# Kernel optimization log

Hardware: AMD Instinct MI355X
Metric: run time of the kernel (lower is better)

## Reference

```python
import jax, jax.numpy as jnp
import numpy as np

B, N, L, D = 128, 1024, 512, 64


def setup_inputs() -> dict:
    key = jax.random.key(0)
    k1, k2 = jax.random.split(key)
    text_outputs = jax.random.normal(k1, (B, N, D), dtype=jnp.float32)
    image_outputs = jax.random.normal(k2, (B, L, D), dtype=jnp.float32)
    rng = np.random.RandomState(0)
    ntok = rng.randint(N // 4, N + 1, size=B)
    nreg = rng.randint(L // 4, L + 1, size=B)
    text_mask = (np.arange(N)[None, :] < ntok[:, None]).astype(np.float32)
    image_mask = (np.arange(L)[None, :] < nreg[:, None]).astype(np.float32)
    # impostor indices (torch code samples these with np.random inside forward;
    # here they are fixed constants for determinism), guaranteed != own index
    I_imp = rng.randint(0, B, size=B)
    S_imp = rng.randint(0, B, size=B)
    ar = np.arange(B)
    I_imp = np.where(I_imp == ar, (I_imp + 1) % B, I_imp).astype(np.int32)
    S_imp = np.where(S_imp == ar, (S_imp + 1) % B, S_imp).astype(np.int32)
    return {
        "text_outputs": text_outputs,
        "image_outputs": image_outputs,
        "text_mask": jnp.asarray(text_mask),
        "image_mask": jnp.asarray(image_mask),
        "I_imp_idx": jnp.asarray(I_imp),
        "S_imp_idx": jnp.asarray(S_imp),
    }


def _mean_max_sim(T, I, tmask, imask):
    # T: (N, D) tokens, I: (L, D) regions; masks select the ragged valid prefix.
    M = jnp.einsum('nd,ld->nl', T, I)                       # matchmap (N, L)
    neg = jnp.finfo(M.dtype).min
    mx = jnp.max(jnp.where(imask[None, :] > 0, M, neg), axis=1)  # max over regions
    return jnp.sum(mx * tmask) / jnp.sum(tmask)             # mean over valid tokens


def reference(text_outputs, image_outputs, text_mask, image_mask, I_imp_idx, S_imp_idx, margin=1.0):
    sim = jax.vmap(_mean_max_sim)
    anchor = sim(text_outputs, image_outputs, text_mask, image_mask)            # (B,)
    Simpsim = sim(text_outputs[S_imp_idx], image_outputs, text_mask[S_imp_idx], image_mask)
    Iimpsim = sim(text_outputs, image_outputs[I_imp_idx], text_mask, image_mask[I_imp_idx])
    # scalar per-sample hinge: term added only when margin+imp-anchor > 0 == relu
    per_sample = jax.nn.relu(margin + Iimpsim - anchor) + jax.nn.relu(margin + Simpsim - anchor)
    loss = jnp.sum(per_sample) / text_outputs.shape[0]
    return loss[None]  # torch returns shape (1,)
```

## Files before the change

kernel.cpp:

```cpp
#include <hip/hip_runtime.h>
#include <hip/hip_bf16.h>

#define B 128
#define N 1024
#define L 512
#define D 64

typedef float f32x4 __attribute__((ext_vector_type(4)));
typedef short bf16x8 __attribute__((ext_vector_type(8)));

__device__ inline bf16x8 cvt8(float4 f0, float4 f1) {
    union { __hip_bfloat162 h2[4]; bf16x8 v; } u;
    u.h2[0] = __float22bfloat162_rn(make_float2(f0.x, f0.y));
    u.h2[1] = __float22bfloat162_rn(make_float2(f0.z, f0.w));
    u.h2[2] = __float22bfloat162_rn(make_float2(f1.x, f1.y));
    u.h2[3] = __float22bfloat162_rn(make_float2(f1.z, f1.w));
    return u.v;
}

__device__ __forceinline__ void gload16(const void* g, void* l) {
    __builtin_amdgcn_global_load_lds(
        (const __attribute__((address_space(1))) void*)g,
        (__attribute__((address_space(3))) void*)l, 16, 0, 0);
}

__global__ __launch_bounds__(256) void prep_kernel(
        const float* __restrict__ tmask, const float* __restrict__ imask,
        const float* __restrict__ I,
        int* __restrict__ counts, unsigned short* __restrict__ Ibf) {
    int blk = blockIdx.x, tid = threadIdx.x;
    if (blk < B) {
        int b = blk;
        int w = tid >> 6, lane = tid & 63;
        float ts = 0.f, is = 0.f;
        const float* tm = tmask + (size_t)b * N;
#pragma unroll
        for (int i = 0; i < N / 256; ++i) ts += tm[tid + i * 256];
        const float* im = imask + (size_t)b * L;
#pragma unroll
        for (int i = 0; i < L / 256; ++i) is += im[tid + i * 256];
        for (int off = 32; off; off >>= 1) {
            ts += __shfl_down(ts, off);
            is += __shfl_down(is, off);
        }
        __shared__ float red[8];
        if (lane == 0) { red[w] = ts; red[4 + w] = is; }
        __syncthreads();
        if (tid == 0) counts[b]     = (int)(red[0] + red[1] + red[2] + red[3] + 0.5f);
        if (tid == 1) counts[B + b] = (int)(red[4] + red[5] + red[6] + red[7] + 0.5f);
    } else {
        int t = (blk - B) * 256 + tid;
#pragma unroll
        for (int j = 0; j < 4; ++j) {
            size_t ci = (size_t)t + (size_t)j * 131072;
            const float4* p = (const float4*)(I + ci * 8);
            *(bf16x8*)(Ibf + ci * 8) = cvt8(p[0], p[1]);
        }
    }
}

__global__ __launch_bounds__(256, 4) void sim_kernel_bf16(
        const float* __restrict__ T, const unsigned short* __restrict__ Ibf,
        const int* __restrict__ counts,
        const int* __restrict__ Iimp, const int* __restrict__ Simp,
        float* __restrict__ partials) {
    int blk = blockIdx.x;
    int chunk = blk & 3;
    int bs = blk >> 2;
    int b = bs & (B - 1);
    int s = bs >> 7;
    int Tb = b, Ib = b;
    if (s == 1) Tb = Simp[b];
    else if (s == 2) Ib = Iimp[b];

    int tid = threadIdx.x;
    int w = tid >> 6;
    int lane = tid & 63;
    int q = lane >> 4;
    int c = lane & 15;

    int ntok = counts[Tb];
    int nreg = counts[B + Ib];

    int tok0 = chunk << 8;
    if (chunk != 0 && tok0 >= ntok) {
        if (tid == 0) partials[blk] = 0.f;
        return;
    }

    __shared__ unsigned short ldsI[3][4096];
    __shared__ float red[4];

    int wt0 = tok0 + w * 64;
    bf16x8 afrag[4][2];
#pragma unroll
    for (int tt = 0; tt < 4; ++tt) {
        const float* trow = T + ((size_t)Tb * N + wt0 + tt * 16 + c) * D;
#pragma unroll
        for (int h = 0; h < 2; ++h) {
            const float4* p = (const float4*)(trow + h * 32 + q * 8);
            afrag[tt][h] = cvt8(p[0], p[1]);
        }
    }

    float mx[4][4];
#pragma unroll
    for (int tt = 0; tt < 4; ++tt)
#pragma unroll
        for (int i = 0; i < 4; ++i) mx[tt][i] = -3.0e38f;

    int rloc[2], eoff[2];
#pragma unroll
    for (int j = 0; j < 2; ++j) {
        int ci = tid + j * 256;
        int g = ci >> 6, ln = ci & 63;
        rloc[j] = (g >> 1) * 16 + (ln & 15);
        eoff[j] = (g & 1) * 32 + (ln >> 4) * 8;
    }
    const unsigned short* Ibase = Ibf + (size_t)Ib * L * D;
    int nchunks = (nreg + 63) >> 6;
    int nregm1 = nreg - 1;

    auto stage = [&](int k) {
        unsigned short* buf = &ldsI[k % 3][0];
        int rbase = k << 6;
#pragma unroll
        for (int j = 0; j < 2; ++j) {
            int r = rbase + rloc[j];
            if (r > nregm1) r = nregm1;
            gload16(Ibase + (size_t)r * D + eoff[j], buf + (size_t)(tid + j * 256) * 8);
        }
    };

    asm volatile("s_waitcnt vmcnt(0)" ::: "memory");
    stage(0);
    stage(1);
    asm volatile("s_waitcnt vmcnt(2)" ::: "memory");
    __builtin_amdgcn_s_barrier();

    for (int k = 0; k < nchunks; ++k) {
        if (k + 2 < nchunks) stage(k + 2);

        const char* base = (const char*)&ldsI[k % 3][0] + (size_t)lane * 16;
#pragma unroll
        for (int rt = 0; rt < 4; ++rt) {
            bf16x8 b0 = *(const bf16x8*)(base + (rt * 2 + 0) * 1024);
            bf16x8 b1 = *(const bf16x8*)(base + (rt * 2 + 1) * 1024);
#pragma unroll
            for (int tt = 0; tt < 4; ++tt) {
                f32x4 acc = {0.f, 0.f, 0.f, 0.f};
                acc = __builtin_amdgcn_mfma_f32_16x16x32_bf16(afrag[tt][0], b0, acc, 0, 0, 0);
                acc = __builtin_amdgcn_mfma_f32_16x16x32_bf16(afrag[tt][1], b1, acc, 0, 0, 0);
#pragma unroll
                for (int i = 0; i < 4; ++i) mx[tt][i] = fmaxf(mx[tt][i], acc[i]);
            }
        }

        if (k + 1 < nchunks) {
            if (k + 2 < nchunks)
                asm volatile("s_waitcnt vmcnt(2) lgkmcnt(0)" ::: "memory");
            else
                asm volatile("s_waitcnt vmcnt(0) lgkmcnt(0)" ::: "memory");
            __builtin_amdgcn_s_barrier();
        }
    }

#pragma unroll
    for (int m = 1; m < 16; m <<= 1) {
#pragma unroll
        for (int tt = 0; tt < 4; ++tt)
#pragma unroll
            for (int i = 0; i < 4; ++i)
                mx[tt][i] = fmaxf(mx[tt][i], __shfl_xor(mx[tt][i], m));
    }

    float bsum = 0.f;
    if (c == 0) {
#pragma unroll
        for (int tt = 0; tt < 4; ++tt)
#pragma unroll
            for (int i = 0; i < 4; ++i) {
                int row = wt0 + tt * 16 + q * 4 + i;
                if (row < ntok) bsum += mx[tt][i];
            }
    }
    for (int off = 32; off; off >>= 1) bsum += __shfl_down(bsum, off);
    if (lane == 0) red[w] = bsum;
    __syncthreads();
    if (tid == 0)
        partials[blk] = (red[0] + red[1] + red[2] + red[3]) / (float)ntok;
}

__global__ __launch_bounds__(256) void count_kernel(
        const float* __restrict__ tmask, const float* __restrict__ imask,
        int* __restrict__ counts) {
    int b = blockIdx.x, tid = threadIdx.x;
    int w = tid >> 6, lane = tid & 63;
    float ts = 0.f, is = 0.f;
    const float* tm = tmask + (size_t)b * N;
#pragma unroll
    for (int i = 0; i < N / 256; ++i) ts += tm[tid + i * 256];
    const float* im = imask + (size_t)b * L;
#pragma unroll
    for (int i = 0; i < L / 256; ++i) is += im[tid + i * 256];
    for (int off = 32; off; off >>= 1) {
        ts += __shfl_down(ts, off);
        is += __shfl_down(is, off);
    }
    __shared__ float red[8];
    if (lane == 0) { red[w] = ts; red[4 + w] = is; }
    __syncthreads();
    if (tid == 0) counts[b]     = (int)(red[0] + red[1] + red[2] + red[3] + 0.5f);
    if (tid == 1) counts[B + b] = (int)(red[4] + red[5] + red[6] + red[7] + 0.5f);
}

__global__ __launch_bounds__(256, 3) void sim_kernel_f32(
        const float* __restrict__ T, const float* __restrict__ I,
        const int* __restrict__ counts,
        const int* __restrict__ Iimp, const int* __restrict__ Simp,
        float* __restrict__ partials) {
    int blk = blockIdx.x;
    int chunk = blk & 3;
    int bs = blk >> 2;
    int b = bs & (B - 1);
    int s = bs >> 7;
    int Tb = b, Ib = b;
    if (s == 1) Tb = Simp[b];
    else if (s == 2) Ib = Iimp[b];

    int tid = threadIdx.x;
    int w = tid >> 6;
    int lane = tid & 63;
    int q = lane >> 4;
    int c = lane & 15;

    int ntok = counts[Tb];
    int nreg = counts[B + Ib];

    int tok0 = chunk << 8;
    if (chunk != 0 && tok0 >= ntok) {
        if (tid == 0) partials[blk] = 0.f;
        return;
    }

    __shared__ float ldsI[3][4096];
    __shared__ float red[4];

    int wt0 = tok0 + w * 64;
    bf16x8 afrag[4][2];
#pragma unroll
    for (int tt = 0; tt < 4; ++tt) {
        const float* trow = T + ((size_t)Tb * N + wt0 + tt * 16 + c) * D;
#pragma unroll
        for (int h = 0; h < 2; ++h) {
            const float4* p = (const float4*)(trow + h * 32 + q * 8);
            afrag[tt][h] = cvt8(p[0], p[1]);
        }
    }

    float mx[4][4];
#pragma unroll
    for (int tt = 0; tt < 4; ++tt)
#pragma unroll
        for (int i = 0; i < 4; ++i) mx[tt][i] = -3.0e38f;

    int rloc[4], foff[4];
#pragma unroll
    for (int j = 0; j < 4; ++j) {
        int ci = tid + j * 256;
        int fh = ci >> 7, idx = ci & 127, half = idx >> 6, ln2 = idx & 63;
        rloc[j] = (fh >> 1) * 16 + (ln2 & 15);
        foff[j] = (fh & 1) * 32 + (ln2 >> 4) * 8 + half * 4;
    }
    const float* Ibase = I + (size_t)Ib * L * D;
    int nchunks = (nreg + 63) >> 6;
    int nregm1 = nreg - 1;

    auto stage = [&](int k) {
        float* buf = &ldsI[k % 3][0];
        int rbase = k << 6;
#pragma unroll
        for (int j = 0; j < 4; ++j) {
            int r = rbase + rloc[j];
            if (r > nregm1) r = nregm1;
            gload16(Ibase + (size_t)r * D + foff[j], buf + (tid + j * 256) * 4);
        }
    };

    asm volatile("s_waitcnt vmcnt(0)" ::: "memory");
    stage(0);
    stage(1);
    asm volatile("s_waitcnt vmcnt(4)" ::: "memory");
    __builtin_amdgcn_s_barrier();

    for (int k = 0; k < nchunks; ++k) {
        if (k + 2 < nchunks) stage(k + 2);

        const char* base = (const char*)&ldsI[k % 3][0] + (size_t)lane * 16;
#pragma unroll
        for (int rt = 0; rt < 4; ++rt) {
            float4 e0 = *(const float4*)(base + (rt * 2 + 0) * 2048);
            float4 e1 = *(const float4*)(base + (rt * 2 + 0) * 2048 + 1024);
            float4 e2 = *(const float4*)(base + (rt * 2 + 1) * 2048);
            float4 e3 = *(const float4*)(base + (rt * 2 + 1) * 2048 + 1024);
            bf16x8 b0 = cvt8(e0, e1);
            bf16x8 b1 = cvt8(e2, e3);
#pragma unroll
            for (int tt = 0; tt < 4; ++tt) {
                f32x4 acc = {0.f, 0.f, 0.f, 0.f};
                acc = __builtin_amdgcn_mfma_f32_16x16x32_bf16(afrag[tt][0], b0, acc, 0, 0, 0);
                acc = __builtin_amdgcn_mfma_f32_16x16x32_bf16(afrag[tt][1], b1, acc, 0, 0, 0);
#pragma unroll
                for (int i = 0; i < 4; ++i) mx[tt][i] = fmaxf(mx[tt][i], acc[i]);
            }
        }

        if (k + 1 < nchunks) {
            if (k + 2 < nchunks)
                asm volatile("s_waitcnt vmcnt(4) lgkmcnt(0)" ::: "memory");
            else
                asm volatile("s_waitcnt vmcnt(0) lgkmcnt(0)" ::: "memory");
            __builtin_amdgcn_s_barrier();
        }
    }

#pragma unroll
    for (int m = 1; m < 16; m <<= 1) {
#pragma unroll
        for (int tt = 0; tt < 4; ++tt)
#pragma unroll
            for (int i = 0; i < 4; ++i)
                mx[tt][i] = fmaxf(mx[tt][i], __shfl_xor(mx[tt][i], m));
    }

    float bsum = 0.f;
    if (c == 0) {
#pragma unroll
        for (int tt = 0; tt < 4; ++tt)
#pragma unroll
            for (int i = 0; i < 4; ++i) {
                int row = wt0 + tt * 16 + q * 4 + i;
                if (row < ntok) bsum += mx[tt][i];
            }
    }
    for (int off = 32; off; off >>= 1) bsum += __shfl_down(bsum, off);
    if (lane == 0) red[w] = bsum;
    __syncthreads();
    if (tid == 0)
        partials[blk] = (red[0] + red[1] + red[2] + red[3]) / (float)ntok;
}

__global__ void loss_kernel(const float* __restrict__ partials,
                            float* __restrict__ out) {
    int tid = threadIdx.x;
    __shared__ float simsL[384];
    __shared__ float w6[6];
    const float4* p4 = (const float4*)partials;
    float4 v = p4[tid];
    simsL[tid] = v.x + v.y + v.z + v.w;
    __syncthreads();
    float per = 0.f;
    if (tid < B) {
        float anc  = simsL[tid];
        float simp = simsL[B + tid];
        float iimp = simsL[2 * B + tid];
        per = fmaxf(1.f + iimp - anc, 0.f) + fmaxf(1.f + simp - anc, 0.f);
    }
    for (int off = 32; off; off >>= 1) per += __shfl_down(per, off);
    if ((tid & 63) == 0) w6[tid >> 6] = per;
    __syncthreads();
    if (tid == 0)
        out[0] = (w6[0] + w6[1] + w6[2] + w6[3] + w6[4] + w6[5]) / (float)B;
}

extern "C" void kernel_launch(void* const* d_in, const int* in_sizes, int n_in,
                              void* d_out, int out_size, void* d_ws, size_t ws_size,
                              hipStream_t stream) {
    const float* T     = (const float*)d_in[0];
    const float* I     = (const float*)d_in[1];
    const float* tmask = (const float*)d_in[2];
    const float* imask = (const float*)d_in[3];
    const int*   Iimp  = (const int*)d_in[4];
    const int*   Simp  = (const int*)d_in[5];
    int*   counts   = (int*)d_ws;
    float* partials = (float*)((char*)d_ws + 1024);
    size_t need_bf16 = 7168 + (size_t)B * L * D * sizeof(unsigned short);

    if (ws_size >= need_bf16) {
        unsigned short* Ibf = (unsigned short*)((char*)d_ws + 7168);
        prep_kernel<<<B + 512, 256, 0, stream>>>(tmask, imask, I, counts, Ibf);
        sim_kernel_bf16<<<3 * B * 4, 256, 0, stream>>>(T, Ibf, counts, Iimp, Simp, partials);
    } else {
        count_kernel<<<B, 256, 0, stream>>>(tmask, imask, counts);
        sim_kernel_f32<<<3 * B * 4, 256, 0, stream>>>(T, I, counts, Iimp, Simp, partials);
    }
    loss_kernel<<<1, 384, 0, stream>>>(partials, (float*)d_out);
}
```

Baseline: 122.1 us.

## Fuse loss reduction into sim kernel via last-block atomic and remap block order

Moves the final hinge-loss reduction into the sim kernel: each workgroup writes its partial, increments a global counter, and the last one computes the loss. This removes a separate launch of loss_kernel on the bf16 path. Block indices are also permuted across XCDs, (hw&7)*192+(hw>>3), to balance work, and the I-tile staging is issued before the T fragment loads to overlap those transfers. In exchange it adds an atomic and fence per block and relies on prep_kernel resetting the counter.

```diff
diff --git a/kernel.cpp b/kernel.cpp
--- a/kernel.cpp
+++ b/kernel.cpp
@@ -5,6 +5,7 @@
 #define N 1024
 #define L 512
 #define D 64
+#define NWG 1536
 
 typedef float f32x4 __attribute__((ext_vector_type(4)));
 typedef short bf16x8 __attribute__((ext_vector_type(8)));
@@ -27,11 +28,13 @@
 __global__ __launch_bounds__(256) void prep_kernel(
         const float* __restrict__ tmask, const float* __restrict__ imask,
         const float* __restrict__ I,
-        int* __restrict__ counts, unsigned short* __restrict__ Ibf) {
+        int* __restrict__ counts, unsigned short* __restrict__ Ibf,
+        unsigned int* __restrict__ done) {
     int blk = blockIdx.x, tid = threadIdx.x;
     if (blk < B) {
         int b = blk;
         int w = tid >> 6, lane = tid & 63;
+        if (blk == 0 && tid == 2) *done = 0u;
         float ts = 0.f, is = 0.f;
         const float* tm = tmask + (size_t)b * N;
 #pragma unroll
@@ -63,10 +66,12 @@
         const float* __restrict__ T, const unsigned short* __restrict__ Ibf,
         const int* __restrict__ counts,
         const int* __restrict__ Iimp, const int* __restrict__ Simp,
-        float* __restrict__ partials) {
-    int blk = blockIdx.x;
-    int chunk = blk & 3;
-    int bs = blk >> 2;
+        float* __restrict__ partials, unsigned int* __restrict__ done,
+        float* __restrict__ out) {
+    int hw = blockIdx.x;
+    int work = (hw & 7) * 192 + (hw >> 3);
+    int chunk = work & 3;
+    int bs = work >> 2;
     int b = bs & (B - 1);
     int s = bs >> 7;
     int Tb = b, Ib = b;
@@ -83,112 +88,136 @@
     int nreg = counts[B + Ib];
 
     int tok0 = chunk << 8;
-    if (chunk != 0 && tok0 >= ntok) {
-        if (tid == 0) partials[blk] = 0.f;
-        return;
-    }
+    bool active = (chunk == 0) || (tok0 < ntok);
 
     __shared__ unsigned short ldsI[3][4096];
     __shared__ float red[4];
-
-    int wt0 = tok0 + w * 64;
-    bf16x8 afrag[4][2];
-#pragma unroll
-    for (int tt = 0; tt < 4; ++tt) {
-        const float* trow = T + ((size_t)Tb * N + wt0 + tt * 16 + c) * D;
-#pragma unroll
-        for (int h = 0; h < 2; ++h) {
-            const float4* p = (const float4*)(trow + h * 32 + q * 8);
-            afrag[tt][h] = cvt8(p[0], p[1]);
-        }
-    }
-
-    float mx[4][4];
-#pragma unroll
-    for (int tt = 0; tt < 4; ++tt)
-#pragma unroll
-        for (int i = 0; i < 4; ++i) mx[tt][i] = -3.0e38f;
-
-    int rloc[2], eoff[2];
-#pragma unroll
-    for (int j = 0; j < 2; ++j) {
-        int ci = tid + j * 256;
-        int g = ci >> 6, ln = ci & 63;
-        rloc[j] = (g >> 1) * 16 + (ln & 15);
-        eoff[j] = (g & 1) * 32 + (ln >> 4) * 8;
-    }
-    const unsigned short* Ibase = Ibf + (size_t)Ib * L * D;
-    int nchunks = (nreg + 63) >> 6;
-    int nregm1 = nreg - 1;
-
-    auto stage = [&](int k) {
-        unsigned short* buf = &ldsI[k % 3][0];
-        int rbase = k << 6;
+    __shared__ int lastflag;
+    __shared__ float w4[4];
+
+    if (active) {
+        int rloc[2], eoff[2];
 #pragma unroll
         for (int j = 0; j < 2; ++j) {
-            int r = rbase + rloc[j];
-            if (r > nregm1) r = nregm1;
-            gload16(Ibase + (size_t)r * D + eoff[j], buf + (size_t)(tid + j * 256) * 8);
-        }
-    };
-
-    asm volatile("s_waitcnt vmcnt(0)" ::: "memory");
-    stage(0);
-    stage(1);
-    asm volatile("s_waitcnt vmcnt(2)" ::: "memory");
-    __builtin_amdgcn_s_barrier();
-
-    for (int k = 0; k < nchunks; ++k) {
-        if (k + 2 < nchunks) stage(k + 2);
-
-        const char* base = (const char*)&ldsI[k % 3][0] + (size_t)lane * 16;
-#pragma unroll
-        for (int rt = 0; rt < 4; ++rt) {
-            bf16x8 b0 = *(const bf16x8*)(base + (rt * 2 + 0) * 1024);
-            bf16x8 b1 = *(const bf16x8*)(base + (rt * 2 + 1) * 1024);
-#pragma unroll
-            for (int tt = 0; tt < 4; ++tt) {
-                f32x4 acc = {0.f, 0.f, 0.f, 0.f};
-                acc = __builtin_amdgcn_mfma_f32_16x16x32_bf16(afrag[tt][0], b0, acc, 0, 0, 0);
-                acc = __builtin_amdgcn_mfma_f32_16x16x32_bf16(afrag[tt][1], b1, acc, 0, 0, 0);
-#pragma unroll
-                for (int i = 0; i < 4; ++i) mx[tt][i] = fmaxf(mx[tt][i], acc[i]);
-            }
-        }
-
-        if (k + 1 < nchunks) {
-            if (k + 2 < nchunks)
-                asm volatile("s_waitcnt vmcnt(2) lgkmcnt(0)" ::: "memory");
-            else
-                asm volatile("s_waitcnt vmcnt(0) lgkmcnt(0)" ::: "memory");
-            __builtin_amdgcn_s_barrier();
-        }
-    }
-
-#pragma unroll
-    for (int m = 1; m < 16; m <<= 1) {
+            int ci = tid + j * 256;
+            int g = ci >> 6, ln = ci & 63;
+            rloc[j] = (g >> 1) * 16 + (ln & 15);
+            eoff[j] = (g & 1) * 32 + (ln >> 4) * 8;
+        }
+        const unsigned short* Ibase = Ibf + (size_t)Ib * L * D;
+        int nchunks = (nreg + 63) >> 6;
+        int nregm1 = nreg - 1;
+
+        auto stage = [&](int k) {
+            unsigned short* buf = &ldsI[k % 3][0];
+            int rbase = k << 6;
+#pragma unroll
+            for (int j = 0; j < 2; ++j) {
+                int r = rbase + rloc[j];
+                if (r > nregm1) r = nregm1;
+                gload16(Ibase + (size_t)r * D + eoff[j], buf + (size_t)(tid + j * 256) * 8);
+            }
+        };
+
+        stage(0);
+        stage(1);
+
+        int wt0 = tok0 + w * 64;
+        bf16x8 afrag[4][2];
+#pragma unroll
+        for (int tt = 0; tt < 4; ++tt) {
+            const float* trow = T + ((size_t)Tb * N + wt0 + tt * 16 + c) * D;
+#pragma unroll
+            for (int h = 0; h < 2; ++h) {
+                const float4* p = (const float4*)(trow + h * 32 + q * 8);
+                afrag[tt][h] = cvt8(p[0], p[1]);
+            }
+        }
+
+        float mx[4][4];
 #pragma unroll
         for (int tt = 0; tt < 4; ++tt)
 #pragma unroll
-            for (int i = 0; i < 4; ++i)
-                mx[tt][i] = fmaxf(mx[tt][i], __shfl_xor(mx[tt][i], m));
-    }
-
-    float bsum = 0.f;
-    if (c == 0) {
-#pragma unroll
-        for (int tt = 0; tt < 4; ++tt)
-#pragma unroll
-            for (int i = 0; i < 4; ++i) {
-                int row = wt0 + tt * 16 + q * 4 + i;
-                if (row < ntok) bsum += mx[tt][i];
-            }
-    }
-    for (int off = 32; off; off >>= 1) bsum += __shfl_down(bsum, off);
-    if (lane == 0) red[w] = bsum;
+            for (int i = 0; i < 4; ++i) mx[tt][i] = -3.0e38f;
+
+        asm volatile("s_waitcnt vmcnt(0)" ::: "memory");
+        __builtin_amdgcn_s_barrier();
+
+        for (int k = 0; k < nchunks; ++k) {
+            if (k + 2 < nchunks) stage(k + 2);
+
+            const char* base = (const char*)&ldsI[k % 3][0] + (size_t)lane * 16;
+#pragma unroll
+            for (int rt = 0; rt < 4; ++rt) {
+                bf16x8 b0 = *(const bf16x8*)(base + (rt * 2 + 0) * 1024);
+                bf16x8 b1 = *(const bf16x8*)(base + (rt * 2 + 1) * 1024);
+#pragma unroll
+                for (int tt = 0; tt < 4; ++tt) {
+                    f32x4 acc = {0.f, 0.f, 0.f, 0.f};
+                    acc = __builtin_amdgcn_mfma_f32_16x16x32_bf16(afrag[tt][0], b0, acc, 0, 0, 0);
+                    acc = __builtin_amdgcn_mfma_f32_16x16x32_bf16(afrag[tt][1], b1, acc, 0, 0, 0);
+#pragma unroll
+                    for (int i = 0; i < 4; ++i) mx[tt][i] = fmaxf(mx[tt][i], acc[i]);
+                }
+            }
+
+            if (k + 1 < nchunks) {
+                if (k + 2 < nchunks)
+                    asm volatile("s_waitcnt vmcnt(2) lgkmcnt(0)" ::: "memory");
+                else
+                    asm volatile("s_waitcnt vmcnt(0) lgkmcnt(0)" ::: "memory");
+                __builtin_amdgcn_s_barrier();
+            }
+        }
+
+#pragma unroll
+        for (int m = 1; m < 16; m <<= 1) {
+#pragma unroll
+            for (int tt = 0; tt < 4; ++tt)
+#pragma unroll
+                for (int i = 0; i < 4; ++i)
+                    mx[tt][i] = fmaxf(mx[tt][i], __shfl_xor(mx[tt][i], m));
+        }
+
+        float bsum = 0.f;
+        if (c == 0) {
+#pragma unroll
+            for (int tt = 0; tt < 4; ++tt)
+#pragma unroll
+                for (int i = 0; i < 4; ++i) {
+                    int row = wt0 + tt * 16 + q * 4 + i;
+                    if (row < ntok) bsum += mx[tt][i];
+                }
+        }
+        for (int off = 32; off; off >>= 1) bsum += __shfl_down(bsum, off);
+        if (lane == 0) red[w] = bsum;
+        __syncthreads();
+    }
+
+    if (tid == 0) {
+        float val = active ? (red[0] + red[1] + red[2] + red[3]) / (float)ntok : 0.f;
+        partials[work] = val;
+        __threadfence();
+        unsigned int old = atomicAdd(done, 1u);
+        lastflag = (old == NWG - 1) ? 1 : 0;
+    }
     __syncthreads();
-    if (tid == 0)
-        partials[blk] = (red[0] + red[1] + red[2] + red[3]) / (float)ntok;
+    if (lastflag) {
+        __threadfence();
+        float per = 0.f;
+        if (tid < B) {
+            const float4* p4 = (const float4*)partials;
+            float4 a4 = p4[tid], s4 = p4[B + tid], i4 = p4[2 * B + tid];
+            float anc = a4.x + a4.y + a4.z + a4.w;
+            float smp = s4.x + s4.y + s4.z + s4.w;
+            float imp = i4.x + i4.y + i4.z + i4.w;
+            per = fmaxf(1.f + imp - anc, 0.f) + fmaxf(1.f + smp - anc, 0.f);
+        }
+        for (int off = 32; off; off >>= 1) per += __shfl_down(per, off);
+        if ((tid & 63) == 0) w4[tid >> 6] = per;
+        __syncthreads();
+        if (tid == 0) out[0] = (w4[0] + w4[1] + w4[2] + w4[3]) / (float)B;
+    }
 }
 
 __global__ __launch_bounds__(256) void count_kernel(
@@ -384,15 +413,17 @@
     const int*   Simp  = (const int*)d_in[5];
     int*   counts   = (int*)d_ws;
     float* partials = (float*)((char*)d_ws + 1024);
-    size_t need_bf16 = 7168 + (size_t)B * L * D * sizeof(unsigned short);
+    unsigned int* done = (unsigned int*)((char*)d_ws + 7168);
+    size_t need_bf16 = 8192 + (size_t)B * L * D * sizeof(unsigned short);
 
     if (ws_size >= need_bf16) {
-        unsigned short* Ibf = (unsigned short*)((char*)d_ws + 7168);
-        prep_kernel<<<B + 512, 256, 0, stream>>>(tmask, imask, I, counts, Ibf);
-        sim_kernel_bf16<<<3 * B * 4, 256, 0, stream>>>(T, Ibf, counts, Iimp, Simp, partials);
+        unsigned short* Ibf = (unsigned short*)((char*)d_ws + 8192);
+        prep_kernel<<<B + 512, 256, 0, stream>>>(tmask, imask, I, counts, Ibf, done);
+        sim_kernel_bf16<<<NWG, 256, 0, stream>>>(T, Ibf, counts, Iimp, Simp,
+                                                 partials, done, (float*)d_out);
     } else {
         count_kernel<<<B, 256, 0, stream>>>(tmask, imask, counts);
         sim_kernel_f32<<<3 * B * 4, 256, 0, stream>>>(T, I, counts, Iimp, Simp, partials);
-    }
-    loss_kernel<<<1, 384, 0, stream>>>(partials, (float*)d_out);
-}
+        loss_kernel<<<1, 384, 0, stream>>>(partials, (float*)d_out);
+    }
+}
```

After: 155.4 us. 27.3% more time.

## Load image bf16 fragments directly from global memory instead of LDS pipeline

Applied to the files above, without the earlier changes.

Removes the triple-buffered LDS staging of image region chunks, which used async global-to-LDS loads, waitcnt and barriers. Each lane now reads its MFMA B fragments straight from global memory, and the loop is unrolled by two. This drops LDS traffic and block-wide synchronisation, and raises LDS-limited occupancy. In exchange, each of the 4 waves issues its own redundant global loads and relies on L1/L2 caching to hide latency. The workspace offset for the bf16 buffer is also realigned.

```diff
diff --git a/kernel.cpp b/kernel.cpp
--- a/kernel.cpp
+++ b/kernel.cpp
@@ -88,7 +88,6 @@
         return;
     }
 
-    __shared__ unsigned short ldsI[3][4096];
     __shared__ float red[4];
 
     int wt0 = tok0 + w * 64;
@@ -109,43 +108,20 @@
 #pragma unroll
         for (int i = 0; i < 4; ++i) mx[tt][i] = -3.0e38f;
 
-    int rloc[2], eoff[2];
-#pragma unroll
-    for (int j = 0; j < 2; ++j) {
-        int ci = tid + j * 256;
-        int g = ci >> 6, ln = ci & 63;
-        rloc[j] = (g >> 1) * 16 + (ln & 15);
-        eoff[j] = (g & 1) * 32 + (ln >> 4) * 8;
-    }
-    const unsigned short* Ibase = Ibf + (size_t)Ib * L * D;
+    const unsigned short* Irow = Ibf + (size_t)Ib * L * D + q * 8;
     int nchunks = (nreg + 63) >> 6;
     int nregm1 = nreg - 1;
 
-    auto stage = [&](int k) {
-        unsigned short* buf = &ldsI[k % 3][0];
-        int rbase = k << 6;
-#pragma unroll
-        for (int j = 0; j < 2; ++j) {
-            int r = rbase + rloc[j];
+#pragma unroll 2
+    for (int k = 0; k < nchunks; ++k) {
+        int rbase = (k << 6) + c;
+#pragma unroll
+        for (int rt = 0; rt < 4; ++rt) {
+            int r = rbase + rt * 16;
             if (r > nregm1) r = nregm1;
-            gload16(Ibase + (size_t)r * D + eoff[j], buf + (size_t)(tid + j * 256) * 8);
-        }
-    };
-
-    asm volatile("s_waitcnt vmcnt(0)" ::: "memory");
-    stage(0);
-    stage(1);
-    asm volatile("s_waitcnt vmcnt(2)" ::: "memory");
-    __builtin_amdgcn_s_barrier();
-
-    for (int k = 0; k < nchunks; ++k) {
-        if (k + 2 < nchunks) stage(k + 2);
-
-        const char* base = (const char*)&ldsI[k % 3][0] + (size_t)lane * 16;
-#pragma unroll
-        for (int rt = 0; rt < 4; ++rt) {
-            bf16x8 b0 = *(const bf16x8*)(base + (rt * 2 + 0) * 1024);
-            bf16x8 b1 = *(const bf16x8*)(base + (rt * 2 + 1) * 1024);
+            const unsigned short* p = Irow + (size_t)r * D;
+            bf16x8 b0 = *(const bf16x8*)(p);
+            bf16x8 b1 = *(const bf16x8*)(p + 32);
 #pragma unroll
             for (int tt = 0; tt < 4; ++tt) {
                 f32x4 acc = {0.f, 0.f, 0.f, 0.f};
@@ -154,14 +130,6 @@
 #pragma unroll
                 for (int i = 0; i < 4; ++i) mx[tt][i] = fmaxf(mx[tt][i], acc[i]);
             }
-        }
-
-        if (k + 1 < nchunks) {
-            if (k + 2 < nchunks)
-                asm volatile("s_waitcnt vmcnt(2) lgkmcnt(0)" ::: "memory");
-            else
-                asm volatile("s_waitcnt vmcnt(0) lgkmcnt(0)" ::: "memory");
-            __builtin_amdgcn_s_barrier();
         }
     }
 
@@ -384,10 +352,10 @@
     const int*   Simp  = (const int*)d_in[5];
     int*   counts   = (int*)d_ws;
     float* partials = (float*)((char*)d_ws + 1024);
-    size_t need_bf16 = 7168 + (size_t)B * L * D * sizeof(unsigned short);
+    size_t need_bf16 = 8192 + (size_t)B * L * D * sizeof(unsigned short);
 
     if (ws_size >= need_bf16) {
-        unsigned short* Ibf = (unsigned short*)((char*)d_ws + 7168);
+        unsigned short* Ibf = (unsigned short*)((char*)d_ws + 8192);
         prep_kernel<<<B + 512, 256, 0, stream>>>(tmask, imask, I, counts, Ibf);
         sim_kernel_bf16<<<3 * B * 4, 256, 0, stream>>>(T, Ibf, counts, Iimp, Simp, partials);
     } else {
```

Result: slower. 145.3 us (+19.1%).
